# Optimization experiments

Hardware: AMD Instinct MI355X
Metric: run time of the kernel (lower is better)

The kernel has to match this reference:

```python
import jax, jax.numpy as jnp
import numpy as np

N_ATTR = 100000   # rows of ndata (node attribute table)
MAX_Z = 100000    # config['max_z']
ATTR_DIM = 64
HID = 32          # hidden_units
NUM_LAYERS = 3
K = 30            # SortPooling k
B = 1024          # number of graphs in the batch
NPG = 256         # nodes per graph
N = B * NPG       # 262144 total nodes
EPG = 4096        # edges per graph
E = B * EPG       # 4194304 total edges
D_LAT = HID * NUM_LAYERS + 1  # 97
DENSE_DIM = (((K - 2) // 2 + 1) - 5 + 1) * 32  # 352


def setup_inputs() -> dict:
    key = jax.random.key(0)
    ks = jax.random.split(key, 24)
    # edges confined within each subgraph (batched graph structure)
    offs = jnp.repeat(jnp.arange(B, dtype=jnp.int32) * NPG, EPG)
    src = offs + jax.random.randint(ks[0], (E,), 0, NPG, dtype=jnp.int32)
    dst = offs + jax.random.randint(ks[1], (E,), 0, NPG, dtype=jnp.int32)
    node_id = jax.random.randint(ks[2], (N,), 0, min(N_ATTR, MAX_Z))
    feats = jax.random.randint(ks[3], (N,), 0, 1000)  # structural z-labels
    edge_id = jax.random.randint(ks[4], (E,), 0, E)
    ndata = jax.random.normal(ks[5], (N_ATTR, ATTR_DIM), jnp.float32)
    edata = jax.random.uniform(ks[6], (E, 1), jnp.float32)
    node_emb = jax.random.normal(ks[7], (N_ATTR + MAX_Z, HID), jnp.float32) * 0.1
    s = 0.05
    d_in = ATTR_DIM + 2 * HID  # 128
    W0 = jax.random.normal(ks[8], (d_in, HID), jnp.float32) * s
    W1 = jax.random.normal(ks[9], (HID, HID), jnp.float32) * s
    W2 = jax.random.normal(ks[10], (HID, HID), jnp.float32) * s
    W3 = jax.random.normal(ks[11], (HID, 1), jnp.float32) * s
    b0 = jnp.zeros((HID,), jnp.float32)
    b1 = jnp.zeros((HID,), jnp.float32)
    b2 = jnp.zeros((HID,), jnp.float32)
    b3 = jnp.zeros((1,), jnp.float32)
    conv1_w = jax.random.normal(ks[12], (16, 1, D_LAT), jnp.float32) * s
    conv1_b = jnp.zeros((16,), jnp.float32)
    conv2_w = jax.random.normal(ks[13], (32, 16, 5), jnp.float32) * s
    conv2_b = jnp.zeros((32,), jnp.float32)
    fc1_w = jax.random.normal(ks[14], (128, DENSE_DIM), jnp.float32) * s
    fc1_b = jnp.zeros((128,), jnp.float32)
    fc2_w = jax.random.normal(ks[15], (1, 128), jnp.float32) * s
    fc2_b = jnp.zeros((1,), jnp.float32)
    return dict(feats=feats, node_id=node_id, edge_id=edge_id, src=src, dst=dst,
                ndata=ndata, edata=edata, node_emb=node_emb,
                W0=W0, b0=b0, W1=W1, b1=b1, W2=W2, b2=b2, W3=W3, b3=b3,
                conv1_w=conv1_w, conv1_b=conv1_b, conv2_w=conv2_w, conv2_b=conv2_b,
                fc1_w=fc1_w, fc1_b=fc1_b, fc2_w=fc2_w, fc2_b=fc2_b)


def _dgcnn_forward(feats, node_id, edge_id, src, dst, ndata, edata, node_emb,
                   W0, b0, W1, b1, W2, b2, W3, b3,
                   conv1_w, conv1_b, conv2_w, conv2_b, fc1_w, fc1_b, fc2_w, fc2_b):
    # --- input features: 3-way embedding concat ---
    x = jnp.concatenate([ndata[node_id], node_emb[feats],
                         node_emb[N_ATTR + node_id]], axis=1)  # [N, 128]
    ew = edata[edge_id][:, 0]  # [E] edge weights
    # DGL GraphConv norm='both': unweighted degree normalization, clamp(min=1)
    ones = jnp.ones((E,), jnp.float32)
    deg_out = jnp.clip(jax.ops.segment_sum(ones, src, num_segments=N), 1.0)
    deg_in = jnp.clip(jax.ops.segment_sum(ones, dst, num_segments=N), 1.0)
    ns = (deg_out ** -0.5)[:, None]  # src norm
    nd = (deg_in ** -0.5)[:, None]   # dst norm

    def gconv(h, W, b):
        # out = D_in^{-1/2} * scatter_add(dst, (D_out^{-1/2} h)[src] * ew) @ W + b
        m = (h * ns)[src] * ew[:, None]                       # [E, d]
        agg = jax.ops.segment_sum(m, dst, num_segments=N)     # [N, d]
        return jnp.tanh((agg * nd) @ W + b)

    h1 = gconv(x, W0, b0)    # [N, 32]
    h2 = gconv(h1, W1, b1)   # [N, 32]
    h3 = gconv(h2, W2, b2)   # [N, 32]
    h4 = gconv(h3, W3, b3)   # [N, 1]
    feat = jnp.concatenate([h1, h2, h3, h4], axis=-1)  # [N, 97]

    # --- SortPooling (DGL): sort each node's features ascending along feature
    # dim, then take top-K nodes per graph sorted descending by last feature ---
    fs = jnp.sort(feat, axis=-1).reshape(B, NPG, D_LAT)
    keys = fs[:, :, -1]                                  # [B, NPG]
    _, idx = jax.lax.top_k(keys, K)                      # [B, K]
    pooled = jnp.take_along_axis(fs, idx[:, :, None], axis=1)  # [B, K, 97]
    z = pooled.reshape(B, 1, K * D_LAT)                  # [B, 1, 2910]

    # --- CNN: Conv1d(1,16,97,stride 97) -> ReLU -> MaxPool(2,2) -> Conv1d(16,32,5) -> ReLU ---
    dn = ('NCH', 'OIH', 'NCH')
    z = jax.lax.conv_general_dilated(z, conv1_w, (D_LAT,), 'VALID', dimension_numbers=dn)
    z = jax.nn.relu(z + conv1_b[None, :, None])          # [B, 16, 30]
    z = jax.lax.reduce_window(z, -jnp.inf, jax.lax.max, (1, 1, 2), (1, 1, 2), 'VALID')  # [B,16,15]
    z = jax.lax.conv_general_dilated(z, conv2_w, (1,), 'VALID', dimension_numbers=dn)
    z = jax.nn.relu(z + conv2_b[None, :, None])          # [B, 32, 11]

    # --- MLP (dropout is identity in eval) ---
    z = z.reshape(B, -1)                                 # [B, 352]
    z = jax.nn.relu(z @ fc1_w.T + fc1_b)
    return z @ fc2_w.T + fc2_b                           # [B, 1]


def reference(feats, node_id, edge_id, src, dst, ndata, edata, node_emb,
              W0, b0, W1, b1, W2, b2, W3, b3,
              conv1_w, conv1_b, conv2_w, conv2_b, fc1_w, fc1_b, fc2_w, fc2_b):
    return _dgcnn_forward(feats, node_id, edge_id, src, dst, ndata, edata, node_emb,
                          W0, b0, W1, b1, W2, b2, W3, b3,
                          conv1_w, conv1_b, conv2_w, conv2_b, fc1_w, fc1_b, fc2_w, fc2_b)
```

## Files before the change

### kernel.cpp

```cpp
#include <hip/hip_runtime.h>
#include <math.h>

#define NPG    256
#define EPG    4096
#define NGRAPH 1024
#define NATTR  100000

#define A_F      0
#define A_YR     102400
#define A_EW     139264
#define A_SRC    155664
#define A_ROWS   159768
#define A_NS     160824
#define A_ND     161848
#define A_BS     162872
#define A_TOTAL  163384

#define E_RAWSD  0
#define E_EWRAW  16384
#define E_DEGI   32768
#define E_DEGO   33792
#define E_CUR    34816

#define H_S30    0
#define H_C1W    12000
#define H_C2W    18208
#define H_L1     28448
#define H_Q      30368
#define H_RR     31328
#define H_FF     32736

__device__ __forceinline__ void aggregate32(const unsigned char* sSrc, const float* sEw,
                                            const int* rowS, const float* Y,
                                            const float* nd, const float* Bs, int boff,
                                            float* F, int t)
{
    #pragma unroll
    for (int r = 0; r < 2; ++r) {
        const int n = r * 128 + (t >> 3);
        const int q = t & 7;
        const int rs = rowS[n], re = rowS[n + 1];
        double a0 = 0.0, a1 = 0.0, a2 = 0.0, a3 = 0.0;
        int   s0 = sSrc[rs];
        float w0 = sEw[rs];
        float4 y0 = *(const float4*)(Y + s0 * 36 + q * 4);
        for (int e = rs; e < re; ++e) {
            const int   s1 = sSrc[e + 1];
            const float w1 = sEw[e + 1];
            const float4 y1 = *(const float4*)(Y + s1 * 36 + q * 4);
            a0 += (double)y0.x * (double)w0;
            a1 += (double)y0.y * (double)w0;
            a2 += (double)y0.z * (double)w0;
            a3 += (double)y0.w * (double)w0;
            y0 = y1; w0 = w1;
        }
        const double sc = (double)nd[n];
        float4 hv;
        hv.x = tanhf((float)(a0 * sc) + Bs[boff + q * 4 + 0]);
        hv.y = tanhf((float)(a1 * sc) + Bs[boff + q * 4 + 1]);
        hv.z = tanhf((float)(a2 * sc) + Bs[boff + q * 4 + 2]);
        hv.w = tanhf((float)(a3 * sc) + Bs[boff + q * 4 + 3]);
        *(float4*)(F + n * 100 + boff + q * 4) = hv;
    }
}

extern "C" __global__ void __launch_bounds__(1024)
dgcnn_fused(const int* __restrict__ feats, const int* __restrict__ node_id,
            const int* __restrict__ edge_id, const int* __restrict__ src,
            const int* __restrict__ dst,
            const float* __restrict__ ndata, const float* __restrict__ edata,
            const float* __restrict__ node_emb,
            const float* __restrict__ W0, const float* __restrict__ b0,
            const float* __restrict__ W1, const float* __restrict__ b1,
            const float* __restrict__ W2, const float* __restrict__ b2,
            const float* __restrict__ W3, const float* __restrict__ b3,
            const float* __restrict__ c1w, const float* __restrict__ c1b,
            const float* __restrict__ c2w, const float* __restrict__ c2b,
            const float* __restrict__ f1w, const float* __restrict__ f1b,
            const float* __restrict__ f2w, const float* __restrict__ f2b,
            float* __restrict__ out)
{
    extern __shared__ char smem[];
    float* F   = (float*)(smem + A_F);
    char*  YRc = smem + A_YR;
    float* Y   = (float*)YRc;
    float* sEw = (float*)(smem + A_EW);
    unsigned char* sSrc = (unsigned char*)(smem + A_SRC);
    int*   rowS = (int*)(smem + A_ROWS);
    float* ns   = (float*)(smem + A_NS);
    float* nd   = (float*)(smem + A_ND);
    float* Bs   = (float*)(smem + A_BS);

    uint*  rawSD = (uint*)(YRc + E_RAWSD);
    float* ewRaw = (float*)(YRc + E_EWRAW);
    int*   degI  = (int*)(YRc + E_DEGI);
    int*   degO  = (int*)(YRc + E_DEGO);
    int*   cur   = (int*)(YRc + E_CUR);

    const int g = blockIdx.x, t = threadIdx.x;
    const int lane = t & 63, wv = t >> 6;

    if (t < NPG) { degI[t] = 0; degO[t] = 0; }
    if (t < 97) Bs[t] = (t < 32) ? b0[t] : (t < 64) ? b1[t - 32]
                       : (t < 96) ? b2[t - 64] : b3[0];
    if (t < 4) { sSrc[4096 + t] = 0; sEw[4096 + t] = 0.f; }
    __syncthreads();
    for (int e = t; e < EPG; e += 1024) {
        const int ge = g * EPG + e;
        const int s = src[ge] - g * NPG;
        const int d = dst[ge] - g * NPG;
        rawSD[e] = (uint)s | ((uint)d << 16);
        ewRaw[e] = edata[edge_id[ge]];
        atomicAdd(&degO[s], 1);
        atomicAdd(&degI[d], 1);
    }
    __syncthreads();
    if (t < NPG) rowS[t + 1] = degI[t];
    if (t == 0)  rowS[0] = 0;
    __syncthreads();
    for (int off = 1; off < NPG; off <<= 1) {
        int add = 0;
        if (t < NPG && t >= off) add = rowS[t + 1 - off];
        __syncthreads();
        if (t < NPG && t >= off) rowS[t + 1] += add;
        __syncthreads();
    }
    if (t < NPG) {
        ns[t] = (float)(1.0 / sqrt((double)(degO[t] > 0 ? degO[t] : 1)));
        nd[t] = (float)(1.0 / sqrt((double)(degI[t] > 0 ? degI[t] : 1)));
        cur[t] = rowS[t];
    }
    __syncthreads();
    for (int e = t; e < EPG; e += 1024) {
        const uint sd = rawSD[e];
        const int d = (int)(sd >> 16), s = (int)(sd & 0xffffu);
        const int pos = atomicAdd(&cur[d], 1);
        sSrc[pos] = (unsigned char)s;
        sEw[pos]  = ewRaw[e];
    }
    __syncthreads();

    const int j = t & 31, nb = t >> 5;

    {
        float acc[8] = {0.f, 0.f, 0.f, 0.f, 0.f, 0.f, 0.f, 0.f};
        for (int c = 0; c < 4; ++c) {
            for (int i = t; i < 2048; i += 1024) {
                const int n = i >> 3, q = i & 7;
                const int gn = g * NPG + n;
                const int nidn = node_id[gn];
                const int j0 = c * 32 + q * 4;
                float4 v;
                if (j0 < 64)      v = *(const float4*)(ndata    + (size_t)nidn * 64 + j0);
                else if (j0 < 96) v = *(const float4*)(node_emb + (size_t)feats[gn] * 32 + (j0 - 64));
                else              v = *(const float4*)(node_emb + (size_t)(NATTR + nidn) * 32 + (j0 - 96));
                const float sc = ns[n];
                float4 o; o.x = v.x * sc; o.y = v.y * sc; o.z = v.z * sc; o.w = v.w * sc;
                *(float4*)(Y + n * 36 + q * 4) = o;
            }
            __syncthreads();
            float wc[32];
            #pragma unroll
            for (int d = 0; d < 32; ++d) wc[d] = W0[(c * 32 + d) * 32 + j];
            #pragma unroll
            for (int i2 = 0; i2 < 8; ++i2) {
                const int n = nb * 8 + i2;
                const float4* ar = (const float4*)(Y + n * 36);
                float a = acc[i2];
                #pragma unroll
                for (int d8 = 0; d8 < 8; ++d8) {
                    const float4 av = ar[d8];
                    a = fmaf(av.x, wc[4 * d8 + 0], a);
                    a = fmaf(av.y, wc[4 * d8 + 1], a);
                    a = fmaf(av.z, wc[4 * d8 + 2], a);
                    a = fmaf(av.w, wc[4 * d8 + 3], a);
                }
                acc[i2] = a;
            }
            __syncthreads();
        }
        #pragma unroll
        for (int i2 = 0; i2 < 8; ++i2) Y[(nb * 8 + i2) * 36 + j] = acc[i2];
        __syncthreads();
        aggregate32(sSrc, sEw, rowS, Y, nd, Bs, 0, F, t);
        __syncthreads();
    }

    for (int L = 0; L < 2; ++L) {
        const float* WL = L ? W2 : W1;
        const int pb = L ? 32 : 0;
        float wc[32];
        #pragma unroll
        for (int d = 0; d < 32; ++d) wc[d] = WL[d * 32 + j];
        float acc[8];
        #pragma unroll
        for (int i2 = 0; i2 < 8; ++i2) {
            const int n = nb * 8 + i2;
            const float4* fr = (const float4*)(F + n * 100 + pb);
            float a = 0.f;
            #pragma unroll
            for (int d8 = 0; d8 < 8; ++d8) {
                const float4 av = fr[d8];
                a = fmaf(av.x, wc[4 * d8 + 0], a);
                a = fmaf(av.y, wc[4 * d8 + 1], a);
                a = fmaf(av.z, wc[4 * d8 + 2], a);
                a = fmaf(av.w, wc[4 * d8 + 3], a);
            }
            acc[i2] = a * ns[n];
        }
        #pragma unroll
        for (int i2 = 0; i2 < 8; ++i2) Y[(nb * 8 + i2) * 36 + j] = acc[i2];
        __syncthreads();
        aggregate32(sSrc, sEw, rowS, Y, nd, Bs, 32 + L * 32, F, t);
        __syncthreads();
    }

    if (t < NPG) {
        const float4* fr = (const float4*)(F + t * 100 + 64);
        float a = 0.f;
        #pragma unroll
        for (int d8 = 0; d8 < 8; ++d8) {
            const float4 h = fr[d8];
            a = fmaf(h.x, W3[4 * d8 + 0], a);
            a = fmaf(h.y, W3[4 * d8 + 1], a);
            a = fmaf(h.z, W3[4 * d8 + 2], a);
            a = fmaf(h.w, W3[4 * d8 + 3], a);
        }
        Y[t] = a * ns[t];
    }
    __syncthreads();
    {
        const int n = t >> 2, p = t & 3;
        const int rs = rowS[n], re = rowS[n + 1];
        double a = 0.0;
        for (int e = rs + p; e < re; e += 4)
            a += (double)sEw[e] * (double)Y[sSrc[e]];
        a += __shfl_xor(a, 1, 64);
        a += __shfl_xor(a, 2, 64);
        if (p == 0)
            F[n * 100 + 96] = tanhf((float)(a * (double)nd[n]) + Bs[96]);
    }
    __syncthreads();

    float* keys = (float*)(smem + A_SRC);
    int*   selI = (int*)(smem + A_SRC + 1024);
    float* S30  = (float*)(YRc + H_S30);
    float* c1wS = (float*)(YRc + H_C1W);
    float* c2wS = (float*)(YRc + H_C2W);
    float* L1   = (float*)(YRc + H_L1);
    float* Q    = (float*)(YRc + H_Q);
    float* Rr   = (float*)(YRc + H_RR);
    float* Ff   = (float*)(YRc + H_FF);

    if (t < NPG) {
        const float* fr = F + t * 100;
        float m0 = fr[0], m1 = fr[1], m2 = fr[2], m3 = fr[3];
        for (int d = 4; d < 96; d += 4) {
            m0 = fmaxf(m0, fr[d]);     m1 = fmaxf(m1, fr[d + 1]);
            m2 = fmaxf(m2, fr[d + 2]); m3 = fmaxf(m3, fr[d + 3]);
        }
        keys[t] = fmaxf(fmaxf(fmaxf(m0, m1), fmaxf(m2, m3)), fr[96]);
    }
    __syncthreads();

    if (t < 64) {
        float kv[4]; int ki[4];
        #pragma unroll
        for (int r = 0; r < 4; ++r) { ki[r] = lane * 4 + r; kv[r] = keys[lane * 4 + r]; }
        for (int it = 0; it < 30; ++it) {
            float bv = kv[0]; int bi = ki[0];
            #pragma unroll
            for (int r = 1; r < 4; ++r)
                if (kv[r] > bv || (kv[r] == bv && ki[r] < bi)) { bv = kv[r]; bi = ki[r]; }
            #pragma unroll
            for (int off = 1; off <= 32; off <<= 1) {
                const float ov = __shfl_xor(bv, off, 64);
                const int   oi = __shfl_xor(bi, off, 64);
                if (ov > bv || (ov == bv && oi < bi)) { bv = ov; bi = oi; }
            }
            if (lane == 0) selI[it] = bi;
            if ((bi >> 2) == lane) kv[bi & 3] = -INFINITY;
        }
    } else {
        for (int i = t - 64; i < 1552; i += 960) c1wS[i] = c1w[i];
        for (int i = t - 64; i < 2560; i += 960) c2wS[i] = c2w[i];
    }
    __syncthreads();

    for (int k = wv; k < 30; k += 16) {
        const float* fr = F + selI[k] * 100;
        float v0 = fr[lane];
        float v1 = (lane < 33) ? fr[64 + lane] : INFINITY;
        for (int kk = 2; kk <= 128; kk <<= 1) {
            for (int jj = kk >> 1; jj > 0; jj >>= 1) {
                if (jj == 64) {
                    const float lo = fminf(v0, v1), hi = fmaxf(v0, v1);
                    v0 = lo; v1 = hi;
                } else {
                    const float p0 = __shfl_xor(v0, jj, 64);
                    const float p1 = __shfl_xor(v1, jj, 64);
                    const bool up   = ((lane & jj) == 0);
                    const bool asc0 = (kk == 128) ? true : ((lane & kk) == 0);
                    const bool asc1 = (kk == 128) ? true : (((64 + lane) & kk) == 0);
                    v0 = (up == asc0) ? fminf(v0, p0) : fmaxf(v0, p0);
                    v1 = (up == asc1) ? fminf(v1, p1) : fmaxf(v1, p1);
                }
            }
        }
        S30[k * 100 + lane] = v0;
        if (lane < 33) S30[k * 100 + 64 + lane] = v1;
    }
    __syncthreads();

    if (t < 480) {
        const int k = t >> 4, c = t & 15;
        const float* row  = S30 + k * 100;
        const float* wrow = c1wS + c * 97;
        float acc = c1b[c];
        for (int d = 0; d < 97; ++d) acc = fmaf(row[d], wrow[d], acc);
        L1[k * 16 + c] = fmaxf(acc, 0.f);
    }
    __syncthreads();
    if (t < 240) {
        const int c = t / 15, tt = t % 15;
        Q[c * 15 + tt] = fmaxf(L1[(2 * tt) * 16 + c], L1[(2 * tt + 1) * 16 + c]);
    }
    __syncthreads();
    if (t < 352) {
        const int o = t / 11, tt = t % 11;
        const float* wo = c2wS + o * 80;
        float acc = c2b[o];
        #pragma unroll
        for (int c = 0; c < 16; ++c)
            #pragma unroll
            for (int jj = 0; jj < 5; ++jj)
                acc = fmaf(Q[c * 15 + tt + jj], wo[c * 5 + jj], acc);
        Rr[o * 11 + tt] = fmaxf(acc, 0.f);
    }
    __syncthreads();
    if (t < 128) {
        float acc = f1b[t];
        const float* wr = f1w + t * 352;
        for (int i = 0; i < 352; ++i) acc = fmaf(Rr[i], wr[i], acc);
        Ff[t] = fmaxf(acc, 0.f);
    }
    __syncthreads();
    if (t < 64) {
        float acc = Ff[lane] * f2w[lane] + Ff[lane + 64] * f2w[lane + 64];
        #pragma unroll
        for (int off = 1; off <= 32; off <<= 1) acc += __shfl_xor(acc, off, 64);
        if (lane == 0) out[g] = acc + f2b[0];
    }
}

extern "C" void kernel_launch(void* const* d_in, const int* in_sizes, int n_in,
                              void* d_out, int out_size, void* d_ws, size_t ws_size,
                              hipStream_t stream)
{
    const int*   feats    = (const int*)d_in[0];
    const int*   node_id  = (const int*)d_in[1];
    const int*   edge_id  = (const int*)d_in[2];
    const int*   src      = (const int*)d_in[3];
    const int*   dst      = (const int*)d_in[4];
    const float* ndata    = (const float*)d_in[5];
    const float* edata    = (const float*)d_in[6];
    const float* node_emb = (const float*)d_in[7];
    const float* W0 = (const float*)d_in[8];
    const float* b0 = (const float*)d_in[9];
    const float* W1 = (const float*)d_in[10];
    const float* b1 = (const float*)d_in[11];
    const float* W2 = (const float*)d_in[12];
    const float* b2 = (const float*)d_in[13];
    const float* W3 = (const float*)d_in[14];
    const float* b3 = (const float*)d_in[15];
    const float* c1w = (const float*)d_in[16];
    const float* c1b = (const float*)d_in[17];
    const float* c2w = (const float*)d_in[18];
    const float* c2b = (const float*)d_in[19];
    const float* f1w = (const float*)d_in[20];
    const float* f1b = (const float*)d_in[21];
    const float* f2w = (const float*)d_in[22];
    const float* f2b = (const float*)d_in[23];

    (void)hipFuncSetAttribute((const void*)dgcnn_fused,
                              hipFuncAttributeMaxDynamicSharedMemorySize, A_TOTAL);

    dgcnn_fused<<<NGRAPH, 1024, A_TOTAL, stream>>>(feats, node_id, edge_id, src, dst,
                                                   ndata, edata, node_emb,
                                                   W0, b0, W1, b1, W2, b2, W3, b3,
                                                   c1w, c1b, c2w, c2b,
                                                   f1w, f1b, f2w, f2b,
                                                   (float*)d_out);
}
```

Baseline: 416.5 us.

## Move node features and CSR edges to global memory to shrink LDS footprint

The full per-graph feature matrix F and the CSR edge list now live in global scratch buffers instead of LDS. LDS use drops from about 163KB to about 80KB, so two blocks can share a CU. Layer outputs are pre-scaled and written into a small LDS ping buffer, and the max-key reduction is folded into the aggregation. The prefix scan becomes a wave-shuffle scan. The cost is global-memory traffic for edge reads during every aggregation and for writing F, and edge src/dst are re-read from global memory.

```diff
diff --git a/kernel.cpp b/kernel.cpp
--- a/kernel.cpp
+++ b/kernel.cpp
@@ -6,21 +6,23 @@
 #define NGRAPH 1024
 #define NATTR  100000
 
-#define A_F      0
-#define A_YR     102400
-#define A_EW     139264
-#define A_SRC    155664
-#define A_ROWS   159768
-#define A_NS     160824
-#define A_ND     161848
-#define A_BS     162872
-#define A_TOTAL  163384
-
-#define E_RAWSD  0
-#define E_EWRAW  16384
-#define E_DEGI   32768
-#define E_DEGO   33792
-#define E_CUR    34816
+__device__ float g_F[(size_t)NGRAPH * NPG * 100];
+__device__ uint2 g_edges[(size_t)NGRAPH * EPG + 8];
+
+#define A_BUFA   0
+#define A_BUFB   36864
+#define A_ROWS   73728
+#define A_NS     74784
+#define A_ND     75808
+#define A_BS     76832
+#define A_KEYS   77344
+#define A_Y4     78368
+#define A_SEL    79392
+#define A_TOTAL  79520
+
+#define E_DEGI   0
+#define E_DEGO   1024
+#define E_CUR    2048
 
 #define H_S30    0
 #define H_C1W    12000
@@ -30,10 +32,12 @@
 #define H_RR     31328
 #define H_FF     32736
 
-__device__ __forceinline__ void aggregate32(const unsigned char* sSrc, const float* sEw,
+__device__ __forceinline__ void aggregate32(const uint2* __restrict__ gE,
                                             const int* rowS, const float* Y,
-                                            const float* nd, const float* Bs, int boff,
-                                            float* F, int t)
+                                            const float* ns, const float* nd,
+                                            const float* Bs, int boff,
+                                            float* Hout, float* keys,
+                                            float* __restrict__ gFg, int t)
 {
     #pragma unroll
     for (int r = 0; r < 2; ++r) {
@@ -41,18 +45,17 @@
         const int q = t & 7;
         const int rs = rowS[n], re = rowS[n + 1];
         double a0 = 0.0, a1 = 0.0, a2 = 0.0, a3 = 0.0;
-        int   s0 = sSrc[rs];
-        float w0 = sEw[rs];
-        float4 y0 = *(const float4*)(Y + s0 * 36 + q * 4);
+        uint2 e0 = gE[rs];
+        float4 y0 = *(const float4*)(Y + e0.y * 36 + q * 4);
         for (int e = rs; e < re; ++e) {
-            const int   s1 = sSrc[e + 1];
-            const float w1 = sEw[e + 1];
-            const float4 y1 = *(const float4*)(Y + s1 * 36 + q * 4);
-            a0 += (double)y0.x * (double)w0;
-            a1 += (double)y0.y * (double)w0;
-            a2 += (double)y0.z * (double)w0;
-            a3 += (double)y0.w * (double)w0;
-            y0 = y1; w0 = w1;
+            const uint2 e1 = gE[e + 1];
+            const float4 y1 = *(const float4*)(Y + e1.y * 36 + q * 4);
+            const double w = (double)__uint_as_float(e0.x);
+            a0 += (double)y0.x * w;
+            a1 += (double)y0.y * w;
+            a2 += (double)y0.z * w;
+            a3 += (double)y0.w * w;
+            e0 = e1; y0 = y1;
         }
         const double sc = (double)nd[n];
         float4 hv;
@@ -60,11 +63,19 @@
         hv.y = tanhf((float)(a1 * sc) + Bs[boff + q * 4 + 1]);
         hv.z = tanhf((float)(a2 * sc) + Bs[boff + q * 4 + 2]);
         hv.w = tanhf((float)(a3 * sc) + Bs[boff + q * 4 + 3]);
-        *(float4*)(F + n * 100 + boff + q * 4) = hv;
+        *(float4*)(gFg + (size_t)n * 100 + boff + q * 4) = hv;
+        const float s2 = ns[n];
+        float4 o; o.x = hv.x * s2; o.y = hv.y * s2; o.z = hv.z * s2; o.w = hv.w * s2;
+        *(float4*)(Hout + n * 36 + q * 4) = o;
+        float m = fmaxf(fmaxf(hv.x, hv.y), fmaxf(hv.z, hv.w));
+        m = fmaxf(m, __shfl_xor(m, 1, 64));
+        m = fmaxf(m, __shfl_xor(m, 2, 64));
+        m = fmaxf(m, __shfl_xor(m, 4, 64));
+        if (q == 0) keys[n] = fmaxf(keys[n], m);
     }
 }
 
-extern "C" __global__ void __launch_bounds__(1024)
+extern "C" __global__ void __launch_bounds__(1024, 8)
 dgcnn_fused(const int* __restrict__ feats, const int* __restrict__ node_id,
             const int* __restrict__ edge_id, const int* __restrict__ src,
             const int* __restrict__ dst,
@@ -81,50 +92,57 @@
             float* __restrict__ out)
 {
     extern __shared__ char smem[];
-    float* F   = (float*)(smem + A_F);
-    char*  YRc = smem + A_YR;
-    float* Y   = (float*)YRc;
-    float* sEw = (float*)(smem + A_EW);
-    unsigned char* sSrc = (unsigned char*)(smem + A_SRC);
+    float* BufA = (float*)(smem + A_BUFA);
+    float* BufB = (float*)(smem + A_BUFB);
     int*   rowS = (int*)(smem + A_ROWS);
     float* ns   = (float*)(smem + A_NS);
     float* nd   = (float*)(smem + A_ND);
     float* Bs   = (float*)(smem + A_BS);
-
-    uint*  rawSD = (uint*)(YRc + E_RAWSD);
-    float* ewRaw = (float*)(YRc + E_EWRAW);
-    int*   degI  = (int*)(YRc + E_DEGI);
-    int*   degO  = (int*)(YRc + E_DEGO);
-    int*   cur   = (int*)(YRc + E_CUR);
+    float* keys = (float*)(smem + A_KEYS);
+    float* y4   = (float*)(smem + A_Y4);
+    int*   selI = (int*)(smem + A_SEL);
 
     const int g = blockIdx.x, t = threadIdx.x;
     const int lane = t & 63, wv = t >> 6;
-
-    if (t < NPG) { degI[t] = 0; degO[t] = 0; }
+    float* gFg = g_F + (size_t)g * NPG * 100;
+    uint2* gE  = g_edges + (size_t)g * EPG;
+
+    int* degI = (int*)((char*)BufA + E_DEGI);
+    int* degO = (int*)((char*)BufA + E_DEGO);
+    int* cur  = (int*)((char*)BufA + E_CUR);
+    float* ewRaw = BufB;
+
+    if (t < NPG) { degI[t] = 0; degO[t] = 0; keys[t] = -INFINITY; }
     if (t < 97) Bs[t] = (t < 32) ? b0[t] : (t < 64) ? b1[t - 32]
                        : (t < 96) ? b2[t - 64] : b3[0];
-    if (t < 4) { sSrc[4096 + t] = 0; sEw[4096 + t] = 0.f; }
     __syncthreads();
     for (int e = t; e < EPG; e += 1024) {
         const int ge = g * EPG + e;
         const int s = src[ge] - g * NPG;
         const int d = dst[ge] - g * NPG;
-        rawSD[e] = (uint)s | ((uint)d << 16);
         ewRaw[e] = edata[edge_id[ge]];
         atomicAdd(&degO[s], 1);
         atomicAdd(&degI[d], 1);
     }
     __syncthreads();
-    if (t < NPG) rowS[t + 1] = degI[t];
-    if (t == 0)  rowS[0] = 0;
-    __syncthreads();
-    for (int off = 1; off < NPG; off <<= 1) {
-        int add = 0;
-        if (t < NPG && t >= off) add = rowS[t + 1 - off];
-        __syncthreads();
-        if (t < NPG && t >= off) rowS[t + 1] += add;
-        __syncthreads();
-    }
+    if (t < 64) {
+        const int d0 = degI[4 * t], d1 = degI[4 * t + 1],
+                  d2 = degI[4 * t + 2], d3 = degI[4 * t + 3];
+        const int p1 = d0, p2 = p1 + d1, p3 = p2 + d2, p4 = p3 + d3;
+        int s = p4;
+        #pragma unroll
+        for (int off = 1; off <= 32; off <<= 1) {
+            const int o = __shfl_up(s, off, 64);
+            if (lane >= off) s += o;
+        }
+        const int excl = s - p4;
+        rowS[4 * t + 1] = excl + p1;
+        rowS[4 * t + 2] = excl + p2;
+        rowS[4 * t + 3] = excl + p3;
+        rowS[4 * t + 4] = excl + p4;
+        if (t == 0) rowS[0] = 0;
+    }
+    __syncthreads();
     if (t < NPG) {
         ns[t] = (float)(1.0 / sqrt((double)(degO[t] > 0 ? degO[t] : 1)));
         nd[t] = (float)(1.0 / sqrt((double)(degI[t] > 0 ? degI[t] : 1)));
@@ -132,11 +150,11 @@
     }
     __syncthreads();
     for (int e = t; e < EPG; e += 1024) {
-        const uint sd = rawSD[e];
-        const int d = (int)(sd >> 16), s = (int)(sd & 0xffffu);
+        const int ge = g * EPG + e;
+        const int s = src[ge] - g * NPG;
+        const int d = dst[ge] - g * NPG;
         const int pos = atomicAdd(&cur[d], 1);
-        sSrc[pos] = (unsigned char)s;
-        sEw[pos]  = ewRaw[e];
+        gE[pos] = make_uint2(__float_as_uint(ewRaw[e]), (uint)s);
     }
     __syncthreads();
 
@@ -156,7 +174,7 @@
                 else              v = *(const float4*)(node_emb + (size_t)(NATTR + nidn) * 32 + (j0 - 96));
                 const float sc = ns[n];
                 float4 o; o.x = v.x * sc; o.y = v.y * sc; o.z = v.z * sc; o.w = v.w * sc;
-                *(float4*)(Y + n * 36 + q * 4) = o;
+                *(float4*)(BufB + n * 36 + q * 4) = o;
             }
             __syncthreads();
             float wc[32];
@@ -165,7 +183,7 @@
             #pragma unroll
             for (int i2 = 0; i2 < 8; ++i2) {
                 const int n = nb * 8 + i2;
-                const float4* ar = (const float4*)(Y + n * 36);
+                const float4* ar = (const float4*)(BufB + n * 36);
                 float a = acc[i2];
                 #pragma unroll
                 for (int d8 = 0; d8 < 8; ++d8) {
@@ -180,15 +198,14 @@
             __syncthreads();
         }
         #pragma unroll
-        for (int i2 = 0; i2 < 8; ++i2) Y[(nb * 8 + i2) * 36 + j] = acc[i2];
+        for (int i2 = 0; i2 < 8; ++i2) BufB[(nb * 8 + i2) * 36 + j] = acc[i2];
         __syncthreads();
-        aggregate32(sSrc, sEw, rowS, Y, nd, Bs, 0, F, t);
+        aggregate32(gE, rowS, BufB, ns, nd, Bs, 0, BufA, keys, gFg, t);
         __syncthreads();
     }
 
     for (int L = 0; L < 2; ++L) {
         const float* WL = L ? W2 : W1;
-        const int pb = L ? 32 : 0;
         float wc[32];
         #pragma unroll
         for (int d = 0; d < 32; ++d) wc[d] = WL[d * 32 + j];
@@ -196,7 +213,7 @@
         #pragma unroll
         for (int i2 = 0; i2 < 8; ++i2) {
             const int n = nb * 8 + i2;
-            const float4* fr = (const float4*)(F + n * 100 + pb);
+            const float4* fr = (const float4*)(BufA + n * 36);
             float a = 0.f;
             #pragma unroll
             for (int d8 = 0; d8 < 8; ++d8) {
@@ -206,17 +223,18 @@
                 a = fmaf(av.z, wc[4 * d8 + 2], a);
                 a = fmaf(av.w, wc[4 * d8 + 3], a);
             }
-            acc[i2] = a * ns[n];
-        }
-        #pragma unroll
-        for (int i2 = 0; i2 < 8; ++i2) Y[(nb * 8 + i2) * 36 + j] = acc[i2];
+            acc[i2] = a;
+        }
         __syncthreads();
-        aggregate32(sSrc, sEw, rowS, Y, nd, Bs, 32 + L * 32, F, t);
+        #pragma unroll
+        for (int i2 = 0; i2 < 8; ++i2) BufB[(nb * 8 + i2) * 36 + j] = acc[i2];
         __syncthreads();
+        aggregate32(gE, rowS, BufB, ns, nd, Bs, 32 + L * 32, BufA, keys, gFg, t);
+        __syncthreads();
     }
 
     if (t < NPG) {
-        const float4* fr = (const float4*)(F + t * 100 + 64);
+        const float4* fr = (const float4*)(BufA + t * 36);
         float a = 0.f;
         #pragma unroll
         for (int d8 = 0; d8 < 8; ++d8) {
@@ -226,42 +244,35 @@
             a = fmaf(h.z, W3[4 * d8 + 2], a);
             a = fmaf(h.w, W3[4 * d8 + 3], a);
         }
-        Y[t] = a * ns[t];
+        y4[t] = a;
     }
     __syncthreads();
     {
         const int n = t >> 2, p = t & 3;
         const int rs = rowS[n], re = rowS[n + 1];
         double a = 0.0;
-        for (int e = rs + p; e < re; e += 4)
-            a += (double)sEw[e] * (double)Y[sSrc[e]];
+        for (int e = rs + p; e < re; e += 4) {
+            const uint2 ed = gE[e];
+            a += (double)__uint_as_float(ed.x) * (double)y4[ed.y];
+        }
         a += __shfl_xor(a, 1, 64);
         a += __shfl_xor(a, 2, 64);
-        if (p == 0)
-            F[n * 100 + 96] = tanhf((float)(a * (double)nd[n]) + Bs[96]);
-    }
-    __syncthreads();
-
-    float* keys = (float*)(smem + A_SRC);
-    int*   selI = (int*)(smem + A_SRC + 1024);
-    float* S30  = (float*)(YRc + H_S30);
-    float* c1wS = (float*)(YRc + H_C1W);
-    float* c2wS = (float*)(YRc + H_C2W);
-    float* L1   = (float*)(YRc + H_L1);
-    float* Q    = (float*)(YRc + H_Q);
-    float* Rr   = (float*)(YRc + H_RR);
-    float* Ff   = (float*)(YRc + H_FF);
-
-    if (t < NPG) {
-        const float* fr = F + t * 100;
-        float m0 = fr[0], m1 = fr[1], m2 = fr[2], m3 = fr[3];
-        for (int d = 4; d < 96; d += 4) {
-            m0 = fmaxf(m0, fr[d]);     m1 = fmaxf(m1, fr[d + 1]);
-            m2 = fmaxf(m2, fr[d + 2]); m3 = fmaxf(m3, fr[d + 3]);
-        }
-        keys[t] = fmaxf(fmaxf(fmaxf(m0, m1), fmaxf(m2, m3)), fr[96]);
-    }
-    __syncthreads();
+        if (p == 0) {
+            const float h = tanhf((float)(a * (double)nd[n]) + Bs[96]);
+            gFg[(size_t)n * 100 + 96] = h;
+            keys[n] = fmaxf(keys[n], h);
+        }
+    }
+    __syncthreads();
+
+    char*  HB   = (char*)BufA;
+    float* S30  = (float*)(HB + H_S30);
+    float* c1wS = (float*)(HB + H_C1W);
+    float* c2wS = (float*)(HB + H_C2W);
+    float* L1   = (float*)(HB + H_L1);
+    float* Q    = (float*)(HB + H_Q);
+    float* Rr   = (float*)(HB + H_RR);
+    float* Ff   = (float*)(HB + H_FF);
 
     if (t < 64) {
         float kv[4]; int ki[4];
@@ -288,7 +299,7 @@
     __syncthreads();
 
     for (int k = wv; k < 30; k += 16) {
-        const float* fr = F + selI[k] * 100;
+        const float* fr = gFg + (size_t)selI[k] * 100;
         float v0 = fr[lane];
         float v1 = (lane < 33) ? fr[64 + lane] : INFINITY;
         for (int kk = 2; kk <= 128; kk <<= 1) {
```

Result: faster. 390.2 us (-6.3%).
